# Performance work log

Hardware: AMD Instinct MI355X
Metric: run time of the kernel (lower is better)

Reference implementation:

```python
import jax, jax.numpy as jnp
import numpy as np

NBINS = 256

def _equalize_flat(flat):
    # flat: [N, P] int32 pixel values in [0,255], N = B*C channels, P = H*W pixels
    N, P = flat.shape
    hist = jax.vmap(lambda v: jnp.bincount(v, length=NBINS))(flat)  # [N, 256]
    bins = jnp.arange(NBINS, dtype=jnp.int32)
    # last nonzero bin value per channel (PIL: drop last nonzero entry from the step sum)
    last_idx = jnp.max(jnp.where(hist != 0, bins[None, :], -1), axis=1)  # [N]
    last_val = jnp.take_along_axis(hist, last_idx[:, None], axis=1)[:, 0]  # [N]
    step = (P - last_val) // 255  # [N] integer floor div
    safe_step = jnp.maximum(step, 1)
    cs = jnp.cumsum(hist, axis=1)  # [N, 256]
    lut = (cs + (step // 2)[:, None]) // safe_step[:, None]
    # pad left with 0, drop last, clamp to [0,255]
    lut = jnp.concatenate([jnp.zeros((N, 1), lut.dtype), lut[:, :-1]], axis=1)
    lut = jnp.clip(lut, 0, 255)
    eq = jnp.take_along_axis(lut, flat, axis=1)  # [N, P]
    # channels with step==0 pass through unchanged
    return jnp.where((step == 0)[:, None], flat, eq)


def setup_inputs() -> dict:
    key = jax.random.key(0)
    img = jax.random.randint(key, (64, 3, 512, 512), 0, 256).astype(jnp.float32)
    return {"img": img}


def reference(img) -> jnp.ndarray:
    B, C, H, W = img.shape
    flat = img.astype(jnp.int32).reshape(B * C, H * W)
    out = _equalize_flat(flat)
    return out.reshape(B, C, H, W).astype(img.dtype)
```

## Files before the change

### kernel.cpp

```cpp
#include <hip/hip_runtime.h>


#define NBINS 256
#define BPC 4
#define CHUNK 65536
#define NVEC (CHUNK / 4)

typedef float vfloat4 __attribute__((ext_vector_type(4)));

__global__ __launch_bounds__(256) void eq_hist_pack_kernel(
    const float* __restrict__ in, unsigned int* __restrict__ pack,
    unsigned int* __restrict__ phist) {
    __shared__ unsigned int lh[NBINS * 32];
    const int t = threadIdx.x;
    const int copy = t & 31;
    const int chan = blockIdx.x >> 2;
    const int blk  = blockIdx.x & 3;

    for (int i = t; i < NBINS * 32; i += 256) lh[i] = 0u;
    __syncthreads();

    const size_t basev = ((size_t)chan * (size_t)(CHUNK * BPC) +
                          (size_t)blk * CHUNK) >> 2;
    const float4* vin = (const float4*)in + basev;
    unsigned int* pout = pack + basev;

    #pragma unroll 4
    for (int i = t; i < NVEC; i += 256) {
        float4 v = vin[i];
        int ix = min(max((int)v.x, 0), 255);
        int iy = min(max((int)v.y, 0), 255);
        int iz = min(max((int)v.z, 0), 255);
        int iw = min(max((int)v.w, 0), 255);
        atomicAdd(&lh[ix * 32 + copy], 1u);
        atomicAdd(&lh[iy * 32 + copy], 1u);
        atomicAdd(&lh[iz * 32 + copy], 1u);
        atomicAdd(&lh[iw * 32 + copy], 1u);
        pout[i] = (unsigned)ix | ((unsigned)iy << 8) |
                  ((unsigned)iz << 16) | ((unsigned)iw << 24);
    }
    __syncthreads();

    unsigned int s = 0;
    #pragma unroll
    for (int c = 0; c < 32; ++c) s += lh[t * 32 + ((t + c) & 31)];
    phist[(size_t)blockIdx.x * NBINS + t] = s;
}

__global__ __launch_bounds__(256) void eq_lut_apply_kernel(
    const unsigned int* __restrict__ pack, const unsigned int* __restrict__ phist,
    float* __restrict__ out, int P) {
    __shared__ float slut[NBINS * 32];
    __shared__ unsigned int s[NBINS];
    __shared__ int sidx[NBINS];
    const int t = threadIdx.x;
    const int copy = t & 31;
    const int chan = blockIdx.x >> 2;
    const int blk  = blockIdx.x & 3;

    unsigned int h = 0;
    const unsigned int* pb = phist + (size_t)chan * BPC * NBINS;
    #pragma unroll
    for (int b = 0; b < BPC; ++b) h += pb[b * NBINS + t];
    s[t] = h;
    sidx[t] = (h != 0u) ? t : -1;
    __syncthreads();

    for (int off = 128; off > 0; off >>= 1) {
        if (t < off) sidx[t] = max(sidx[t], sidx[t + off]);
        __syncthreads();
    }
    const int last_idx = sidx[0];
    const int last_val = (int)s[last_idx];
    const int step = (P - last_val) / 255;

    for (int off = 1; off < NBINS; off <<= 1) {
        unsigned int v = (t >= off) ? s[t - off] : 0u;
        __syncthreads();
        s[t] += v;
        __syncthreads();
    }

    float lv;
    if (step == 0) {
        lv = (float)t;
    } else {
        int csp = (t == 0) ? 0 : (int)s[t - 1];
        int l = (csp + (step >> 1)) / step;
        lv = (float)min(max(l, 0), 255);
    }
    #pragma unroll
    for (int c = 0; c < 32; ++c)
        slut[t * 32 + ((t + c) & 31)] = lv;
    __syncthreads();

    const size_t basev = ((size_t)chan * (size_t)(CHUNK * BPC) +
                          (size_t)blk * CHUNK) >> 2;
    const unsigned int* pin = pack + basev;
    vfloat4* vout = (vfloat4*)out + basev;

    #pragma unroll 4
    for (int i = t; i < NVEC; i += 256) {
        unsigned int p = pin[i];
        vfloat4 r;
        r.x = slut[(p & 255u) * 32 + copy];
        r.y = slut[((p >> 8) & 255u) * 32 + copy];
        r.z = slut[((p >> 16) & 255u) * 32 + copy];
        r.w = slut[(p >> 24) * 32 + copy];
        __builtin_nontemporal_store(r, &vout[i]);
    }
}

extern "C" void kernel_launch(void* const* d_in, const int* in_sizes, int n_in,
                              void* d_out, int out_size, void* d_ws, size_t ws_size,
                              hipStream_t stream) {
    const float* img = (const float*)d_in[0];
    float* out = (float*)d_out;

    const int P = 512 * 512;
    const int total = in_sizes[0];
    const int N = total / P;

    unsigned int* pack  = (unsigned int*)d_ws;
    unsigned int* phist = (unsigned int*)((char*)d_ws + (size_t)total);

    eq_hist_pack_kernel<<<N * BPC, 256, 0, stream>>>(img, pack, phist);
    eq_lut_apply_kernel<<<N * BPC, 256, 0, stream>>>(pack, phist, out, P);
}
```

Measured before the change: 349.1 us.

## Fuse histogram and LUT apply into one cooperative kernel with grid sync

Merges the histogram and LUT-apply passes into a single cooperative kernel that syncs the whole grid after writing per-block partial histograms, then builds the LUT and re-reads the float input to apply it. The packed 8-bit intermediate buffer is dropped, so the byte-pack write and read go away and each block's input chunk may still be in cache on the second read. It relies on all 768 blocks being co-resident for the cooperative launch, and falls back to two kernels that re-read the float input if the launch fails. Re-reading float input costs more bandwidth than reading the packed bytes.

```diff
diff --git a/kernel.cpp b/kernel.cpp
--- a/kernel.cpp
+++ b/kernel.cpp
@@ -1,4 +1,7 @@
 #include <hip/hip_runtime.h>
+#include <hip/hip_cooperative_groups.h>
+
+namespace cg = cooperative_groups;
 
 
 #define NBINS 256
@@ -8,22 +11,21 @@
 
 typedef float vfloat4 __attribute__((ext_vector_type(4)));
 
-__global__ __launch_bounds__(256) void eq_hist_pack_kernel(
-    const float* __restrict__ in, unsigned int* __restrict__ pack,
-    unsigned int* __restrict__ phist) {
+__global__ __launch_bounds__(256) void eq_fused_kernel(
+    const float* __restrict__ in, float* __restrict__ out,
+    unsigned int* __restrict__ phist, int P) {
     __shared__ unsigned int lh[NBINS * 32];
+    __shared__ unsigned int s[NBINS];
+    __shared__ int sidx[NBINS];
     const int t = threadIdx.x;
     const int copy = t & 31;
     const int chan = blockIdx.x >> 2;
-    const int blk  = blockIdx.x & 3;
 
     for (int i = t; i < NBINS * 32; i += 256) lh[i] = 0u;
     __syncthreads();
 
-    const size_t basev = ((size_t)chan * (size_t)(CHUNK * BPC) +
-                          (size_t)blk * CHUNK) >> 2;
+    const size_t basev = ((size_t)blockIdx.x * CHUNK) >> 2;
     const float4* vin = (const float4*)in + basev;
-    unsigned int* pout = pack + basev;
 
     #pragma unroll 4
     for (int i = t; i < NVEC; i += 256) {
@@ -36,19 +38,92 @@
         atomicAdd(&lh[iy * 32 + copy], 1u);
         atomicAdd(&lh[iz * 32 + copy], 1u);
         atomicAdd(&lh[iw * 32 + copy], 1u);
-        pout[i] = (unsigned)ix | ((unsigned)iy << 8) |
-                  ((unsigned)iz << 16) | ((unsigned)iw << 24);
-    }
-    __syncthreads();
-
-    unsigned int s = 0;
-    #pragma unroll
-    for (int c = 0; c < 32; ++c) s += lh[t * 32 + ((t + c) & 31)];
-    phist[(size_t)blockIdx.x * NBINS + t] = s;
+    }
+    __syncthreads();
+
+    unsigned int hsum = 0;
+    #pragma unroll
+    for (int c = 0; c < 32; ++c) hsum += lh[t * 32 + ((t + c) & 31)];
+    phist[(size_t)blockIdx.x * NBINS + t] = hsum;
+
+    cg::this_grid().sync();
+
+    unsigned int h = 0;
+    const unsigned int* pb = phist + (size_t)chan * BPC * NBINS;
+    #pragma unroll
+    for (int b = 0; b < BPC; ++b) h += pb[b * NBINS + t];
+    s[t] = h;
+    sidx[t] = (h != 0u) ? t : -1;
+    __syncthreads();
+
+    for (int off = 128; off > 0; off >>= 1) {
+        if (t < off) sidx[t] = max(sidx[t], sidx[t + off]);
+        __syncthreads();
+    }
+    const int last_idx = sidx[0];
+    const int last_val = (int)s[last_idx];
+    const int step = (P - last_val) / 255;
+
+    for (int off = 1; off < NBINS; off <<= 1) {
+        unsigned int v = (t >= off) ? s[t - off] : 0u;
+        __syncthreads();
+        s[t] += v;
+        __syncthreads();
+    }
+
+    float lv;
+    if (step == 0) {
+        lv = (float)t;
+    } else {
+        int csp = (t == 0) ? 0 : (int)s[t - 1];
+        lv = (float)min(max((csp + (step >> 1)) / step, 0), 255);
+    }
+
+    float* slut = (float*)lh;
+    #pragma unroll
+    for (int c = 0; c < 32; ++c)
+        slut[t * 32 + ((t + c) & 31)] = lv;
+    __syncthreads();
+
+    vfloat4* vout = (vfloat4*)out + basev;
+    #pragma unroll 4
+    for (int i = t; i < NVEC; i += 256) {
+        float4 v = vin[i];
+        vfloat4 r;
+        r.x = slut[min(max((int)v.x, 0), 255) * 32 + copy];
+        r.y = slut[min(max((int)v.y, 0), 255) * 32 + copy];
+        r.z = slut[min(max((int)v.z, 0), 255) * 32 + copy];
+        r.w = slut[min(max((int)v.w, 0), 255) * 32 + copy];
+        __builtin_nontemporal_store(r, &vout[i]);
+    }
+}
+
+__global__ __launch_bounds__(256) void eq_hist_kernel(
+    const float* __restrict__ in, unsigned int* __restrict__ phist) {
+    __shared__ unsigned int lh[NBINS * 32];
+    const int t = threadIdx.x;
+    const int copy = t & 31;
+    for (int i = t; i < NBINS * 32; i += 256) lh[i] = 0u;
+    __syncthreads();
+    const size_t basev = ((size_t)blockIdx.x * CHUNK) >> 2;
+    const float4* vin = (const float4*)in + basev;
+    #pragma unroll 4
+    for (int i = t; i < NVEC; i += 256) {
+        float4 v = vin[i];
+        atomicAdd(&lh[min(max((int)v.x, 0), 255) * 32 + copy], 1u);
+        atomicAdd(&lh[min(max((int)v.y, 0), 255) * 32 + copy], 1u);
+        atomicAdd(&lh[min(max((int)v.z, 0), 255) * 32 + copy], 1u);
+        atomicAdd(&lh[min(max((int)v.w, 0), 255) * 32 + copy], 1u);
+    }
+    __syncthreads();
+    unsigned int hsum = 0;
+    #pragma unroll
+    for (int c = 0; c < 32; ++c) hsum += lh[t * 32 + ((t + c) & 31)];
+    phist[(size_t)blockIdx.x * NBINS + t] = hsum;
 }
 
 __global__ __launch_bounds__(256) void eq_lut_apply_kernel(
-    const unsigned int* __restrict__ pack, const unsigned int* __restrict__ phist,
+    const float* __restrict__ in, const unsigned int* __restrict__ phist,
     float* __restrict__ out, int P) {
     __shared__ float slut[NBINS * 32];
     __shared__ unsigned int s[NBINS];
@@ -56,7 +131,6 @@
     const int t = threadIdx.x;
     const int copy = t & 31;
     const int chan = blockIdx.x >> 2;
-    const int blk  = blockIdx.x & 3;
 
     unsigned int h = 0;
     const unsigned int* pb = phist + (size_t)chan * BPC * NBINS;
@@ -65,7 +139,6 @@
     s[t] = h;
     sidx[t] = (h != 0u) ? t : -1;
     __syncthreads();
-
     for (int off = 128; off > 0; off >>= 1) {
         if (t < off) sidx[t] = max(sidx[t], sidx[t + off]);
         __syncthreads();
@@ -73,40 +146,33 @@
     const int last_idx = sidx[0];
     const int last_val = (int)s[last_idx];
     const int step = (P - last_val) / 255;
-
     for (int off = 1; off < NBINS; off <<= 1) {
         unsigned int v = (t >= off) ? s[t - off] : 0u;
         __syncthreads();
         s[t] += v;
         __syncthreads();
     }
-
     float lv;
-    if (step == 0) {
-        lv = (float)t;
-    } else {
+    if (step == 0) lv = (float)t;
+    else {
         int csp = (t == 0) ? 0 : (int)s[t - 1];
-        int l = (csp + (step >> 1)) / step;
-        lv = (float)min(max(l, 0), 255);
-    }
-    #pragma unroll
-    for (int c = 0; c < 32; ++c)
-        slut[t * 32 + ((t + c) & 31)] = lv;
-    __syncthreads();
-
-    const size_t basev = ((size_t)chan * (size_t)(CHUNK * BPC) +
-                          (size_t)blk * CHUNK) >> 2;
-    const unsigned int* pin = pack + basev;
+        lv = (float)min(max((csp + (step >> 1)) / step, 0), 255);
+    }
+    #pragma unroll
+    for (int c = 0; c < 32; ++c) slut[t * 32 + ((t + c) & 31)] = lv;
+    __syncthreads();
+
+    const size_t basev = ((size_t)blockIdx.x * CHUNK) >> 2;
+    const float4* vin = (const float4*)in + basev;
     vfloat4* vout = (vfloat4*)out + basev;
-
-    #pragma unroll 4
-    for (int i = t; i < NVEC; i += 256) {
-        unsigned int p = pin[i];
+    #pragma unroll 4
+    for (int i = t; i < NVEC; i += 256) {
+        float4 v = vin[i];
         vfloat4 r;
-        r.x = slut[(p & 255u) * 32 + copy];
-        r.y = slut[((p >> 8) & 255u) * 32 + copy];
-        r.z = slut[((p >> 16) & 255u) * 32 + copy];
-        r.w = slut[(p >> 24) * 32 + copy];
+        r.x = slut[min(max((int)v.x, 0), 255) * 32 + copy];
+        r.y = slut[min(max((int)v.y, 0), 255) * 32 + copy];
+        r.z = slut[min(max((int)v.z, 0), 255) * 32 + copy];
+        r.w = slut[min(max((int)v.w, 0), 255) * 32 + copy];
         __builtin_nontemporal_store(r, &vout[i]);
     }
 }
@@ -121,9 +187,14 @@
     const int total = in_sizes[0];
     const int N = total / P;
 
-    unsigned int* pack  = (unsigned int*)d_ws;
-    unsigned int* phist = (unsigned int*)((char*)d_ws + (size_t)total);
-
-    eq_hist_pack_kernel<<<N * BPC, 256, 0, stream>>>(img, pack, phist);
-    eq_lut_apply_kernel<<<N * BPC, 256, 0, stream>>>(pack, phist, out, P);
-}
+    unsigned int* phist = (unsigned int*)d_ws;
+
+    int Pv = P;
+    void* args[] = {(void*)&img, (void*)&out, (void*)&phist, (void*)&Pv};
+    hipError_t err = hipLaunchCooperativeKernel(
+        (const void*)eq_fused_kernel, dim3(N * BPC), dim3(256), args, 0, stream);
+    if (err != hipSuccess) {
+        eq_hist_kernel<<<N * BPC, 256, 0, stream>>>(img, phist);
+        eq_lut_apply_kernel<<<N * BPC, 256, 0, stream>>>(img, phist, out, P);
+    }
+}
```

Result: slower. 453.4 us (+29.9%).
